# Performance work log

Hardware: AMD Instinct MI355X
Metric: run time of the kernel (lower is better)

## Reference

```python
import jax, jax.numpy as jnp
import numpy as np

B, G = 128, 20000
HID = 64
NUM_BINS = 10
LEAKY_SLOPE = 0.01  # torch nn.LeakyReLU default


def setup_inputs() -> dict:
    key = jax.random.key(0)
    k1, k2, k3, k4, k5, k6 = jax.random.split(key, 6)
    vals = jax.random.normal(k1, (B, G), dtype=jnp.float32)
    keep = jax.random.uniform(k2, (B, G)) < 0.1
    expr_value = jnp.where(keep, vals, 0.0)
    # MLP params: Linear(1 -> HID), Linear(HID -> NUM_BINS-1)
    W1 = jax.random.normal(k3, (1, HID), dtype=jnp.float32) * 0.5
    b1 = jax.random.normal(k4, (HID,), dtype=jnp.float32) * 0.1
    W2 = jax.random.normal(k5, (HID, NUM_BINS - 1), dtype=jnp.float32) * (1.0 / np.sqrt(HID))
    b2 = jax.random.normal(k6, (NUM_BINS - 1,), dtype=jnp.float32) * 0.1
    return {"expr_value": expr_value, "W1": W1, "b1": b1, "W2": W2, "b2": b2}


def reference(expr_value, W1, b1, W2, b2):
    # mask of nonzero expression positions (B, G)
    mask_expr = (expr_value != 0).astype(jnp.float32)
    # tiny MLP applied to every position (vectorized; zero positions masked out below)
    x = expr_value[..., None]                      # (B, G, 1)
    h = x * W1[0] + b1                             # (B, G, HID); Linear(1->HID)
    h = jnp.where(h >= 0, h, LEAKY_SLOPE * h)      # LeakyReLU
    logits = jnp.einsum('bgh,hk->bgk', h, W2) + b2 # (B, G, NUM_BINS-1)
    p = jax.nn.softmax(logits, axis=-1)            # softmax over bins 1..num_bins-1
    m = mask_expr[..., None]
    # bin 0 prob = 1 where expr==0 else 0; bins 1.. = softmax where expr!=0 else 0
    probs = jnp.concatenate([1.0 - m, p * m], axis=-1)  # (B, G, NUM_BINS)
    return probs, mask_expr
```

## Files before the change

kernel.cpp:

```cpp
#include <hip/hip_runtime.h>

#define BB 128
#define GG 20000
#define HID 64
#define KB 9
#define NTOT (BB * GG)
#define EPT 4
#define BLOCK 256
#define LEAKY 0.01f

__global__ __launch_bounds__(BLOCK) void expr_quant_kernel(
    const float* __restrict__ expr,
    const float* __restrict__ W1,
    const float* __restrict__ b1,
    const float* __restrict__ W2,
    const float* __restrict__ b2,
    float* __restrict__ out)
{
    __shared__ float sW1[HID];
    __shared__ float sB1[HID];
    __shared__ float sW2[HID * KB];
    __shared__ float sB2[KB];

    const int tid = threadIdx.x;
    if (tid < HID) { sW1[tid] = W1[tid]; sB1[tid] = b1[tid]; }
    for (int t = tid; t < HID * KB; t += BLOCK) sW2[t] = W2[t];
    if (tid < KB) sB2[tid] = b2[tid];
    __syncthreads();

    const int i0 = (blockIdx.x * BLOCK + tid) * EPT;
    const float4 xv = *(const float4*)(expr + i0);
    float x[EPT] = {xv.x, xv.y, xv.z, xv.w};

    float acc[EPT][KB];
    #pragma unroll
    for (int k = 0; k < KB; ++k) {
        const float bk = sB2[k];
        #pragma unroll
        for (int e = 0; e < EPT; ++e) acc[e][k] = bk;
    }

    #pragma unroll 8
    for (int j = 0; j < HID; ++j) {
        const float w1 = sW1[j];
        const float bb = sB1[j];
        float u[EPT];
        #pragma unroll
        for (int e = 0; e < EPT; ++e) {
            const float t = fmaf(x[e], w1, bb);
            u[e] = fmaxf(t, LEAKY * t);
        }
        #pragma unroll
        for (int k = 0; k < KB; ++k) {
            const float w2 = sW2[j * KB + k];
            #pragma unroll
            for (int e = 0; e < EPT; ++e) acc[e][k] = fmaf(u[e], w2, acc[e][k]);
        }
    }

    float o[EPT * 10];
    float msk[EPT];
    #pragma unroll
    for (int e = 0; e < EPT; ++e) {
        float m = acc[e][0];
        #pragma unroll
        for (int k = 1; k < KB; ++k) m = fmaxf(m, acc[e][k]);
        float p[KB];
        float s = 0.f;
        #pragma unroll
        for (int k = 0; k < KB; ++k) { p[k] = __expf(acc[e][k] - m); s += p[k]; }
        const float r = __frcp_rn(s);
        const bool nz = (x[e] != 0.f);
        msk[e] = nz ? 1.f : 0.f;
        o[e * 10 + 0] = nz ? 0.f : 1.f;
        #pragma unroll
        for (int k = 0; k < KB; ++k) o[e * 10 + 1 + k] = nz ? p[k] * r : 0.f;
    }

    float4* dst = (float4*)(out + (size_t)i0 * 10);
    #pragma unroll
    for (int q = 0; q < 10; ++q) dst[q] = ((const float4*)o)[q];

    float4* mdst = (float4*)(out + (size_t)NTOT * 10 + i0);
    *mdst = make_float4(msk[0], msk[1], msk[2], msk[3]);
}

extern "C" void kernel_launch(void* const* d_in, const int* in_sizes, int n_in,
                              void* d_out, int out_size, void* d_ws, size_t ws_size,
                              hipStream_t stream) {
    const float* expr = (const float*)d_in[0];
    const float* W1   = (const float*)d_in[1];
    const float* b1   = (const float*)d_in[2];
    const float* W2   = (const float*)d_in[3];
    const float* b2   = (const float*)d_in[4];
    float* out = (float*)d_out;

    const int nblocks = NTOT / (BLOCK * EPT);
    expr_quant_kernel<<<nblocks, BLOCK, 0, stream>>>(expr, W1, b1, W2, b2, out);
}
```

Measured before the change: 161.6 us.

## Replace per-element MLP with piecewise-linear logit table and binary search

Since the hidden layer is 1-D input through LeakyReLU, the logits are piecewise linear in x with breakpoints at -b1/W1. A setup kernel sorts the 64 breakpoints and precomputes the slope and intercept of each of the 9 logits for all 65 intervals into workspace. The main kernel then does a 7-step binary search per element and 9 FMAs instead of 64x9 FMAs. This adds an extra launch and table load, and a fused fallback is used when the workspace is too small. Values that fall exactly on a breakpoint or with W1==0 rely on sentinel handling.

```diff
diff --git a/kernel.cpp b/kernel.cpp
--- a/kernel.cpp
+++ b/kernel.cpp
@@ -1,88 +1,138 @@
 #include <hip/hip_runtime.h>
+#include <math.h>
 
-#define BB 128
-#define GG 20000
 #define HID 64
 #define KB 9
-#define NTOT (BB * GG)
+#define NB 10
+#define NTOT (128 * 20000)
 #define EPT 4
 #define BLOCK 256
 #define LEAKY 0.01f
+#define RSTRIDE 20
+#define TAB_FLOATS (128 + 65 * RSTRIDE)
+#define WS_BYTES (TAB_FLOATS * 4)
+#define SENT 3.0e38f
 
-__global__ __launch_bounds__(BLOCK) void expr_quant_kernel(
-    const float* __restrict__ expr,
-    const float* __restrict__ W1,
-    const float* __restrict__ b1,
-    const float* __restrict__ W2,
-    const float* __restrict__ b2,
-    float* __restrict__ out)
+__device__ __forceinline__ void build_table(
+    const float* __restrict__ W1, const float* __restrict__ b1,
+    const float* __restrict__ W2, const float* __restrict__ b2,
+    int tid, float* ts , float* tab ,
+    float* st, float* sw, float* sb, float* tsrt)
 {
-    __shared__ float sW1[HID];
-    __shared__ float sB1[HID];
-    __shared__ float sW2[HID * KB];
-    __shared__ float sB2[KB];
+    if (tid < HID) {
+        float w = W1[tid], b = b1[tid];
+        st[tid] = (w != 0.0f) ? (-b / w) : -SENT;
+        sw[tid] = w; sb[tid] = b;
+    }
+    __syncthreads();
+    if (tid < HID) {
+        float t = st[tid];
+        int r = 0;
+        for (int i = 0; i < HID; ++i) {
+            float ti = st[i];
+            r += (ti < t || (ti == t && i < tid)) ? 1 : 0;
+        }
+        tsrt[r] = t;
+    }
+    __syncthreads();
+    if (tid < 128) ts[tid] = (tid < HID) ? tsrt[tid] : SENT;
+    for (int item = tid; item < 65 * KB; item += BLOCK) {
+        int r = item / KB, k = item - r * KB;
+        float xm;
+        if (r == 0)        xm = tsrt[0] - 1.0f;
+        else if (r == HID) xm = tsrt[HID - 1] + 1.0f;
+        else               xm = 0.5f * (tsrt[r - 1] + tsrt[r]);
+        float A = 0.0f, C = b2[k];
+        for (int j = 0; j < HID; ++j) {
+            float w = sw[j], bb = sb[j];
+            float s = (fmaf(w, xm, bb) >= 0.0f) ? 1.0f : LEAKY;
+            float w2s = W2[j * KB + k] * s;
+            A = fmaf(w2s, w, A);
+            C = fmaf(w2s, bb, C);
+        }
+        tab[r * RSTRIDE + k] = A;
+        tab[r * RSTRIDE + KB + k] = C;
+    }
+    __syncthreads();
+}
 
-    const int tid = threadIdx.x;
-    if (tid < HID) { sW1[tid] = W1[tid]; sB1[tid] = b1[tid]; }
-    for (int t = tid; t < HID * KB; t += BLOCK) sW2[t] = W2[t];
-    if (tid < KB) sB2[tid] = b2[tid];
-    __syncthreads();
-
-    const int i0 = (blockIdx.x * BLOCK + tid) * EPT;
+__device__ __forceinline__ void compute_elems(
+    const float* __restrict__ expr, float* __restrict__ out,
+    const float* ts, const float* tab, int i0)
+{
     const float4 xv = *(const float4*)(expr + i0);
     float x[EPT] = {xv.x, xv.y, xv.z, xv.w};
-
-    float acc[EPT][KB];
-    #pragma unroll
-    for (int k = 0; k < KB; ++k) {
-        const float bk = sB2[k];
-        #pragma unroll
-        for (int e = 0; e < EPT; ++e) acc[e][k] = bk;
-    }
-
-    #pragma unroll 8
-    for (int j = 0; j < HID; ++j) {
-        const float w1 = sW1[j];
-        const float bb = sB1[j];
-        float u[EPT];
-        #pragma unroll
-        for (int e = 0; e < EPT; ++e) {
-            const float t = fmaf(x[e], w1, bb);
-            u[e] = fmaxf(t, LEAKY * t);
-        }
-        #pragma unroll
-        for (int k = 0; k < KB; ++k) {
-            const float w2 = sW2[j * KB + k];
-            #pragma unroll
-            for (int e = 0; e < EPT; ++e) acc[e][k] = fmaf(u[e], w2, acc[e][k]);
-        }
-    }
-
-    float o[EPT * 10];
+    float o[EPT * NB];
     float msk[EPT];
     #pragma unroll
     for (int e = 0; e < EPT; ++e) {
-        float m = acc[e][0];
+        const float xe = x[e];
+        int idx = 0;
         #pragma unroll
-        for (int k = 1; k < KB; ++k) m = fmaxf(m, acc[e][k]);
+        for (int s = 64; s >= 1; s >>= 1)
+            idx += (ts[idx + s - 1] <= xe) ? s : 0;
+        const float* row = tab + idx * RSTRIDE;
+        float lg[KB];
+        #pragma unroll
+        for (int k = 0; k < KB; ++k) lg[k] = fmaf(row[k], xe, row[KB + k]);
+        float m = lg[0];
+        #pragma unroll
+        for (int k = 1; k < KB; ++k) m = fmaxf(m, lg[k]);
         float p[KB];
-        float s = 0.f;
+        float s = 0.0f;
         #pragma unroll
-        for (int k = 0; k < KB; ++k) { p[k] = __expf(acc[e][k] - m); s += p[k]; }
+        for (int k = 0; k < KB; ++k) { p[k] = __expf(lg[k] - m); s += p[k]; }
         const float r = __frcp_rn(s);
-        const bool nz = (x[e] != 0.f);
-        msk[e] = nz ? 1.f : 0.f;
-        o[e * 10 + 0] = nz ? 0.f : 1.f;
+        const bool nz = (xe != 0.0f);
+        msk[e] = nz ? 1.0f : 0.0f;
+        o[e * NB] = nz ? 0.0f : 1.0f;
         #pragma unroll
-        for (int k = 0; k < KB; ++k) o[e * 10 + 1 + k] = nz ? p[k] * r : 0.f;
+        for (int k = 0; k < KB; ++k) o[e * NB + 1 + k] = nz ? p[k] * r : 0.0f;
     }
+    float4* dst = (float4*)(out + (size_t)i0 * NB);
+    #pragma unroll
+    for (int q = 0; q < EPT * NB / 4; ++q) dst[q] = ((const float4*)o)[q];
+    float4* mdst = (float4*)(out + (size_t)NTOT * NB + i0);
+    *mdst = make_float4(msk[0], msk[1], msk[2], msk[3]);
+}
 
-    float4* dst = (float4*)(out + (size_t)i0 * 10);
-    #pragma unroll
-    for (int q = 0; q < 10; ++q) dst[q] = ((const float4*)o)[q];
+__global__ __launch_bounds__(BLOCK) void setup_kernel(
+    const float* __restrict__ W1, const float* __restrict__ b1,
+    const float* __restrict__ W2, const float* __restrict__ b2,
+    float* __restrict__ ws)
+{
+    __shared__ float st[HID], sw[HID], sb[HID], tsrt[HID];
+    build_table(W1, b1, W2, b2, threadIdx.x, ws, ws + 128, st, sw, sb, tsrt);
+}
 
-    float4* mdst = (float4*)(out + (size_t)NTOT * 10 + i0);
-    *mdst = make_float4(msk[0], msk[1], msk[2], msk[3]);
+__global__ __launch_bounds__(BLOCK) void main_kernel(
+    const float* __restrict__ expr, const float* __restrict__ ws,
+    float* __restrict__ out)
+{
+    __shared__ float ts[128];
+    __shared__ float tab[65 * RSTRIDE];
+    const int tid = threadIdx.x;
+    for (int t = tid; t < TAB_FLOATS; t += BLOCK) {
+        float v = ws[t];
+        if (t < 128) ts[t] = v; else tab[t - 128] = v;
+    }
+    __syncthreads();
+    const int i0 = (blockIdx.x * BLOCK + tid) * EPT;
+    compute_elems(expr, out, ts, tab, i0);
+}
+
+__global__ __launch_bounds__(BLOCK) void fused_kernel(
+    const float* __restrict__ expr,
+    const float* __restrict__ W1, const float* __restrict__ b1,
+    const float* __restrict__ W2, const float* __restrict__ b2,
+    float* __restrict__ out)
+{
+    __shared__ float ts[128];
+    __shared__ float tab[65 * RSTRIDE];
+    __shared__ float st[HID], sw[HID], sb[HID], tsrt[HID];
+    build_table(W1, b1, W2, b2, threadIdx.x, ts, tab, st, sw, sb, tsrt);
+    const int i0 = (blockIdx.x * BLOCK + threadIdx.x) * EPT;
+    compute_elems(expr, out, ts, tab, i0);
 }
 
 extern "C" void kernel_launch(void* const* d_in, const int* in_sizes, int n_in,
@@ -94,7 +144,13 @@
     const float* W2   = (const float*)d_in[3];
     const float* b2   = (const float*)d_in[4];
     float* out = (float*)d_out;
+    const int nblocks = NTOT / (BLOCK * EPT);
 
-    const int nblocks = NTOT / (BLOCK * EPT);
-    expr_quant_kernel<<<nblocks, BLOCK, 0, stream>>>(expr, W1, b1, W2, b2, out);
+    if (ws_size >= (size_t)WS_BYTES) {
+        float* ws = (float*)d_ws;
+        setup_kernel<<<1, BLOCK, 0, stream>>>(W1, b1, W2, b2, ws);
+        main_kernel<<<nblocks, BLOCK, 0, stream>>>(expr, ws, out);
+    } else {
+        fused_kernel<<<nblocks, BLOCK, 0, stream>>>(expr, W1, b1, W2, b2, out);
+    }
 }
```

New measurement: 154.8 us. 1.04x faster.
